# Kernel tuning notes

Hardware: AMD Instinct MI355X
Metric: run time of the kernel (lower is better)

The kernel has to match this reference:

```python
import jax, jax.numpy as jnp
import numpy as np

N_NODES = 50000


def _sage_conv(x, src, dst, W_l, W_r, b, num_nodes):
    # message = x[src]; scatter-mean onto dst (PyG SAGEConv aggr='mean')
    msg = x[src]                                                # [E, C_in]
    agg_sum = jax.ops.segment_sum(msg, dst, num_segments=num_nodes)
    deg = jax.ops.segment_sum(jnp.ones((src.shape[0],), x.dtype), dst,
                              num_segments=num_nodes)
    agg = agg_sum / jnp.maximum(deg, 1.0)[:, None]              # mean, deg clamped to 1
    # lin_l(agg) + lin_r(x); bias lives in lin_l (PyG default)
    return agg @ W_l.T + x @ W_r.T + b


def setup_inputs() -> dict:
    key = jax.random.key(0)
    ks = jax.random.split(key, 8)
    C = 128
    s = 1.0 / np.sqrt(C)
    x = jax.random.normal(ks[0], (N_NODES, C), dtype=jnp.float32)
    edge_index = jax.random.randint(ks[1], (2, 800000), 0, N_NODES, dtype=jnp.int64)
    W1_l = jax.random.uniform(ks[2], (C, C), jnp.float32, -s, s)
    W1_r = jax.random.uniform(ks[3], (C, C), jnp.float32, -s, s)
    b1 = jax.random.uniform(ks[4], (C,), jnp.float32, -s, s)
    W2_l = jax.random.uniform(ks[5], (C, C), jnp.float32, -s, s)
    W2_r = jax.random.uniform(ks[6], (C, C), jnp.float32, -s, s)
    b2 = jax.random.uniform(ks[7], (C,), jnp.float32, -s, s)
    return {"x": x, "edge_index": edge_index,
            "W1_l": W1_l, "W1_r": W1_r, "b1": b1,
            "W2_l": W2_l, "W2_r": W2_r, "b2": b2}


def reference(x, edge_index, W1_l, W1_r, b1, W2_l, W2_r, b2):
    src, dst = edge_index[0], edge_index[1]
    h = _sage_conv(x, src, dst, W1_l, W1_r, b1, N_NODES)
    h = jax.nn.relu(h)  # dropout p=0.0 -> no-op
    out = _sage_conv(h, src, dst, W2_l, W2_r, b2, N_NODES)
    return out
```

## Files before the change

kernel.cpp:

```cpp
#include <hip/hip_runtime.h>

#define NCH 128
#define MAXBKT 512
#define BKT_SHIFT 7
#define BKT_NODES 128
#define BIN_BATCH 1024
#define NHIST 64

typedef __attribute__((ext_vector_type(8))) short bf16x8;
typedef __attribute__((ext_vector_type(4))) float f32x4;

__device__ __forceinline__ unsigned short f2bf_rne(float f) {
  unsigned u = __float_as_uint(f);
  unsigned r = u + 0x7FFF + ((u >> 16) & 1);
  return (unsigned short)(r >> 16);
}

__device__ __forceinline__ void prepW_elem(const float* __restrict__ Wl,
                                           const float* __restrict__ Wr,
                                           unsigned short* __restrict__ WhiF,
                                           unsigned short* __restrict__ WloF, int i) {
  int kc   = i >> 12;
  int r    = i & 4095;
  int nt   = r >> 9;
  int r2   = r & 511;
  int lane = r2 >> 3;
  int e    = r2 & 7;
  int j = nt * 16 + (lane & 15);
  int k = kc * 32 + (lane >> 4) * 8 + e;
  float w = (k < 128) ? Wl[j * 128 + k] : Wr[j * 128 + (k - 128)];
  unsigned u = __float_as_uint(w);
  float fhi = __uint_as_float(u & 0xFFFF0000u);
  float flo = w - fhi;
  WhiF[i] = (unsigned short)(u >> 16);
  WloF[i] = (unsigned short)(__float_as_uint(flo) >> 16);
}

__global__ __launch_bounds__(256) void k_hist_prep(
    const int* __restrict__ dst, int* __restrict__ partial,
    const float* __restrict__ x, unsigned short* __restrict__ xbf,
    const float* __restrict__ W1l, const float* __restrict__ W1r,
    const float* __restrict__ W2l, const float* __restrict__ W2r,
    unsigned short* __restrict__ W1hi, unsigned short* __restrict__ W1lo,
    unsigned short* __restrict__ W2hi, unsigned short* __restrict__ W2lo,
    int nE, int n8) {
  int t = threadIdx.x;
  if (blockIdx.x < NHIST) {
    __shared__ int h[MAXBKT];
    h[t] = 0; h[t + 256] = 0;
    __syncthreads();
    for (int e = blockIdx.x * 256 + t; e < nE; e += NHIST * 256)
      atomicAdd(&h[dst[e] >> BKT_SHIFT], 1);
    __syncthreads();
    partial[t * NHIST + blockIdx.x] = h[t];
    partial[(t + 256) * NHIST + blockIdx.x] = h[t + 256];
  } else {
    int i = (blockIdx.x - NHIST) * 256 + t;
    if (i < n8) {
      const float4* p = reinterpret_cast<const float4*>(x + (size_t)i * 8);
      float4 v0 = p[0], v1 = p[1];
      uint4 o;
      o.x = (unsigned)f2bf_rne(v0.x) | ((unsigned)f2bf_rne(v0.y) << 16);
      o.y = (unsigned)f2bf_rne(v0.z) | ((unsigned)f2bf_rne(v0.w) << 16);
      o.z = (unsigned)f2bf_rne(v1.x) | ((unsigned)f2bf_rne(v1.y) << 16);
      o.w = (unsigned)f2bf_rne(v1.z) | ((unsigned)f2bf_rne(v1.w) << 16);
      *reinterpret_cast<uint4*>(xbf + (size_t)i * 8) = o;
    } else {
      int j = i - n8;
      if (j < 32768)       prepW_elem(W1l, W1r, W1hi, W1lo, j);
      else if (j < 65536)  prepW_elem(W2l, W2r, W2hi, W2lo, j - 32768);
    }
  }
}

__global__ __launch_bounds__(512) void k_bktscan(const int* __restrict__ partial,
                                                 int* __restrict__ bktBase,
                                                 int* __restrict__ bktCursor, int nBkt) {
  __shared__ int sc[512];
  int t = threadIdx.x;
  int v = 0;
  const int4* p4 = reinterpret_cast<const int4*>(partial + t * NHIST);
#pragma unroll
  for (int b = 0; b < NHIST / 4; b++) {
    int4 d = p4[b];
    v += d.x + d.y + d.z + d.w;
  }
  sc[t] = v;
  __syncthreads();
  for (int off = 1; off < 512; off <<= 1) {
    int u = (t >= off) ? sc[t - off] : 0;
    __syncthreads();
    sc[t] += u;
    __syncthreads();
  }
  bktBase[t] = sc[t] - v;
  if (t == 511) bktBase[512] = sc[511];
  bktCursor[t] = 0;
}

__global__ __launch_bounds__(256) void k_bin(const int* __restrict__ src,
                                             const int* __restrict__ dst,
                                             const int* __restrict__ bktBase,
                                             int* __restrict__ bktCursor,
                                             unsigned* __restrict__ binned,
                                             int nE, int nBkt) {
  __shared__ int hist[MAXBKT];
  __shared__ int boff[MAXBKT];
  int t = threadIdx.x;
  hist[t] = 0; hist[t + 256] = 0;
  __syncthreads();

  int eb = blockIdx.x * BIN_BATCH;
  unsigned pk[4];
  short bkt[4];
  int rk[4];
#pragma unroll
  for (int i = 0; i < 4; i++) {
    int e = eb + t + i * 256;
    if (e < nE) {
      int s = src[e], d = dst[e];
      bkt[i] = (short)(d >> BKT_SHIFT);
      pk[i] = (unsigned)s | ((unsigned)(d & (BKT_NODES - 1)) << 16);
      rk[i] = atomicAdd(&hist[d >> BKT_SHIFT], 1);
    } else rk[i] = -1;
  }
  __syncthreads();
  for (int i = t; i < nBkt; i += 256)
    boff[i] = hist[i] ? atomicAdd(&bktCursor[i], hist[i]) : 0;
  __syncthreads();
#pragma unroll
  for (int i = 0; i < 4; i++) {
    if (rk[i] >= 0) {
      int b = bkt[i];
      binned[bktBase[b] + boff[b] + rk[i]] = pk[i];
    }
  }
}

__global__ __launch_bounds__(256) void k_build(const unsigned* __restrict__ binned,
                                               const int* __restrict__ bktBase,
                                               int* __restrict__ start,
                                               float* __restrict__ invdeg,
                                               int* __restrict__ srcSorted,
                                               int nN, int nE) {
  __shared__ int cnt[BKT_NODES];
  __shared__ int sc[BKT_NODES];
  __shared__ int cur[BKT_NODES];
  int b = blockIdx.x, t = threadIdx.x;
  int base = b << BKT_SHIFT;
  int e0 = bktBase[b], e1 = bktBase[b + 1];

  if (t < BKT_NODES) { cnt[t] = 0; cur[t] = 0; }
  __syncthreads();
  for (int i = e0 + t; i < e1; i += 256)
    atomicAdd(&cnt[binned[i] >> 16], 1);
  __syncthreads();
  if (t < BKT_NODES) sc[t] = cnt[t];
  __syncthreads();
  for (int off = 1; off < BKT_NODES; off <<= 1) {
    int u = (t < BKT_NODES && t >= off) ? sc[t - off] : 0;
    __syncthreads();
    if (t < BKT_NODES && t >= off) sc[t] += u;
    __syncthreads();
  }
  if (t < BKT_NODES) {
    int n = base + t;
    if (n < nN) {
      start[n] = e0 + sc[t] - cnt[t];
      invdeg[n] = 1.0f / fmaxf((float)cnt[t], 1.0f);
    }
  }
  if (b == 0 && t == 0) start[nN] = nE;
  __syncthreads();
  for (int i = e0 + t; i < e1; i += 256) {
    unsigned p = binned[i];
    int ld = p >> 16;
    int pos = e0 + sc[ld] - cnt[ld] + atomicAdd(&cur[ld], 1);
    srcSorted[pos] = (int)(p & 0xFFFFu);
  }
}

#define ACC8(v)                                          \
  a0 += __uint_as_float((v).x << 16);                    \
  a1 += __uint_as_float((v).x & 0xFFFF0000u);            \
  a2 += __uint_as_float((v).y << 16);                    \
  a3 += __uint_as_float((v).y & 0xFFFF0000u);            \
  a4 += __uint_as_float((v).z << 16);                    \
  a5 += __uint_as_float((v).z & 0xFFFF0000u);            \
  a6 += __uint_as_float((v).w << 16);                    \
  a7 += __uint_as_float((v).w & 0xFFFF0000u);

__global__ __launch_bounds__(256) void k_gather(const unsigned short* __restrict__ xbf,
                                                const int* __restrict__ srcSorted,
                                                const int* __restrict__ start,
                                                const float* __restrict__ invdeg,
                                                unsigned short* __restrict__ aggbf,
                                                int nN) {
  int node = (blockIdx.x * 256 + threadIdx.x) >> 6;
  if (node >= nN) return;
  int lane = threadIdx.x & 63;
  int unit = lane >> 4;
  int ul   = lane & 15;
  const unsigned short* xb = xbf + ul * 8;

  int s0 = start[node], s1 = start[node + 1];
  float a0 = 0.f, a1 = 0.f, a2 = 0.f, a3 = 0.f,
        a4 = 0.f, a5 = 0.f, a6 = 0.f, a7 = 0.f;
  int i = s0 + unit;
  for (; i + 12 < s1; i += 16) {
    int sa = srcSorted[i],     sb = srcSorted[i + 4];
    int sc = srcSorted[i + 8], sd = srcSorted[i + 12];
    uint4 va = *reinterpret_cast<const uint4*>(xb + (size_t)sa * NCH);
    uint4 vb = *reinterpret_cast<const uint4*>(xb + (size_t)sb * NCH);
    uint4 vc = *reinterpret_cast<const uint4*>(xb + (size_t)sc * NCH);
    uint4 vd = *reinterpret_cast<const uint4*>(xb + (size_t)sd * NCH);
    ACC8(va) ACC8(vb) ACC8(vc) ACC8(vd)
  }
  for (; i < s1; i += 4) {
    int s = srcSorted[i];
    uint4 v = *reinterpret_cast<const uint4*>(xb + (size_t)s * NCH);
    ACC8(v)
  }
  a0 += __shfl_xor(a0, 16); a0 += __shfl_xor(a0, 32);
  a1 += __shfl_xor(a1, 16); a1 += __shfl_xor(a1, 32);
  a2 += __shfl_xor(a2, 16); a2 += __shfl_xor(a2, 32);
  a3 += __shfl_xor(a3, 16); a3 += __shfl_xor(a3, 32);
  a4 += __shfl_xor(a4, 16); a4 += __shfl_xor(a4, 32);
  a5 += __shfl_xor(a5, 16); a5 += __shfl_xor(a5, 32);
  a6 += __shfl_xor(a6, 16); a6 += __shfl_xor(a6, 32);
  a7 += __shfl_xor(a7, 16); a7 += __shfl_xor(a7, 32);

  if (lane < 16) {
    float idg = invdeg[node];
    uint4 o;
    o.x = (unsigned)f2bf_rne(a0 * idg) | ((unsigned)f2bf_rne(a1 * idg) << 16);
    o.y = (unsigned)f2bf_rne(a2 * idg) | ((unsigned)f2bf_rne(a3 * idg) << 16);
    o.z = (unsigned)f2bf_rne(a4 * idg) | ((unsigned)f2bf_rne(a5 * idg) << 16);
    o.w = (unsigned)f2bf_rne(a6 * idg) | ((unsigned)f2bf_rne(a7 * idg) << 16);
    *reinterpret_cast<uint4*>(aggbf + (size_t)node * NCH + ul * 8) = o;
  }
}

__global__ __launch_bounds__(256, 3) void k_linear_mfma(
    const unsigned short* __restrict__ aggbf, const unsigned short* __restrict__ xinbf,
    const unsigned short* __restrict__ Whi, const unsigned short* __restrict__ Wlo,
    const float* __restrict__ bias, float* __restrict__ outF,
    unsigned short* __restrict__ outBf, int relu, int nNodes) {
  int t = threadIdx.x;
  int wave = t >> 6;
  int lane = t & 63;
  int l15 = lane & 15;
  int lq  = lane >> 4;
  int r0 = (blockIdx.x * 4 + wave) * 32;

  const bf16x8* WhiV = reinterpret_cast<const bf16x8*>(Whi) + lane;
  const bf16x8* WloV = reinterpret_cast<const bf16x8*>(Wlo) + lane;

  f32x4 accA[8], accB[8];
#pragma unroll
  for (int i = 0; i < 8; i++) {
    accA[i] = (f32x4){0.f, 0.f, 0.f, 0.f};
    accB[i] = (f32x4){0.f, 0.f, 0.f, 0.f};
  }

  int rA = r0 + l15;        if (rA >= nNodes) rA = nNodes - 1;
  int rB = r0 + 16 + l15;   if (rB >= nNodes) rB = nNodes - 1;

#pragma unroll
  for (int kc = 0; kc < 8; kc++) {
    const unsigned short* ab = (kc < 4) ? aggbf : xinbf;
    int k128 = (kc & 3) * 32 + lq * 8;
    bf16x8 aA = *reinterpret_cast<const bf16x8*>(ab + (size_t)rA * NCH + k128);
    bf16x8 aB = *reinterpret_cast<const bf16x8*>(ab + (size_t)rB * NCH + k128);
#pragma unroll
    for (int nt = 0; nt < 8; nt++) {
      int fidx = (kc * 8 + nt) * 64;
      bf16x8 bhi = WhiV[fidx];
      bf16x8 blo = WloV[fidx];
      accA[nt] = __builtin_amdgcn_mfma_f32_16x16x32_bf16(aA, bhi, accA[nt], 0, 0, 0);
      accA[nt] = __builtin_amdgcn_mfma_f32_16x16x32_bf16(aA, blo, accA[nt], 0, 0, 0);
      accB[nt] = __builtin_amdgcn_mfma_f32_16x16x32_bf16(aB, bhi, accB[nt], 0, 0, 0);
      accB[nt] = __builtin_amdgcn_mfma_f32_16x16x32_bf16(aB, blo, accB[nt], 0, 0, 0);
    }
  }

#pragma unroll
  for (int nt = 0; nt < 8; nt++) {
    int col = nt * 16 + l15;
    float bv = bias[col];
#pragma unroll
    for (int i = 0; i < 4; i++) {
      int rowA = r0 + lq * 4 + i;
      if (rowA < nNodes) {
        float v = accA[nt][i] + bv;
        if (relu) v = fmaxf(v, 0.f);
        if (outBf) outBf[(size_t)rowA * NCH + col] = f2bf_rne(v);
        else       outF[(size_t)rowA * NCH + col] = v;
      }
      int rowB = r0 + 16 + lq * 4 + i;
      if (rowB < nNodes) {
        float v = accB[nt][i] + bv;
        if (relu) v = fmaxf(v, 0.f);
        if (outBf) outBf[(size_t)rowB * NCH + col] = f2bf_rne(v);
        else       outF[(size_t)rowB * NCH + col] = v;
      }
    }
  }
}

extern "C" void kernel_launch(void* const* d_in, const int* in_sizes, int n_in,
                              void* d_out, int out_size, void* d_ws, size_t ws_size,
                              hipStream_t stream) {
  const float* x   = (const float*)d_in[0];
  const int*   ei  = (const int*)d_in[1];
  const float* W1l = (const float*)d_in[2];
  const float* W1r = (const float*)d_in[3];
  const float* b1  = (const float*)d_in[4];
  const float* W2l = (const float*)d_in[5];
  const float* W2r = (const float*)d_in[6];
  const float* b2  = (const float*)d_in[7];
  float* out = (float*)d_out;

  const int nE = in_sizes[1] / 2;
  const int nN = in_sizes[0] / NCH;
  const int* src = ei;
  const int* dst = ei + nE;
  const int nBkt = (nN + BKT_NODES - 1) >> BKT_SHIFT;

  size_t bfBytes = (size_t)nN * NCH * sizeof(unsigned short);
  size_t wBytes  = (size_t)128 * 256 * sizeof(unsigned short);
  auto align256 = [](size_t v) { return (v + 255) & ~(size_t)255; };

  char* ws = (char*)d_ws;
  unsigned short* xbf   = (unsigned short*)ws;  ws += bfBytes;
  unsigned short* aggbf = (unsigned short*)ws;  ws += bfBytes;
  unsigned short* hbf   = (unsigned short*)ws;  ws += bfBytes;
  unsigned* binned = (unsigned*)ws;             ws += align256((size_t)nE * sizeof(unsigned));
  int*   srcSorted = (int*)ws;                  ws += align256((size_t)nE * sizeof(int));
  int*   startRow  = (int*)ws;                  ws += align256((size_t)(nN + 1) * sizeof(int));
  float* invdeg    = (float*)ws;                ws += align256((size_t)nN * sizeof(float));
  int*   partial   = (int*)ws;                  ws += (size_t)NHIST * MAXBKT * sizeof(int);
  int*   bktCursor = (int*)ws;                  ws += MAXBKT * sizeof(int);
  int*   bktBase   = (int*)ws;                  ws += align256((MAXBKT + 1) * sizeof(int));
  unsigned short* W1hi = (unsigned short*)ws;   ws += wBytes;
  unsigned short* W1lo = (unsigned short*)ws;   ws += wBytes;
  unsigned short* W2hi = (unsigned short*)ws;   ws += wBytes;
  unsigned short* W2lo = (unsigned short*)ws;   ws += wBytes;

  int n8 = nN * NCH / 8;
  int prepBlocks = (n8 + 2 * 32768) / 256;

  k_hist_prep<<<NHIST + prepBlocks, 256, 0, stream>>>(dst, partial, x, xbf,
                                                      W1l, W1r, W2l, W2r,
                                                      W1hi, W1lo, W2hi, W2lo, nE, n8);
  k_bktscan<<<1, 512, 0, stream>>>(partial, bktBase, bktCursor, nBkt);
  k_bin<<<(nE + BIN_BATCH - 1) / BIN_BATCH, 256, 0, stream>>>(src, dst, bktBase,
                                                              bktCursor, binned, nE, nBkt);
  k_build<<<nBkt, 256, 0, stream>>>(binned, bktBase, startRow, invdeg, srcSorted, nN, nE);

  int gatherBlocks = (nN * 64 + 255) / 256;
  int linBlocks = (nN + 127) / 128;

  k_gather<<<gatherBlocks, 256, 0, stream>>>(xbf, srcSorted, startRow, invdeg, aggbf, nN);
  k_linear_mfma<<<linBlocks, 256, 0, stream>>>(aggbf, xbf, W1hi, W1lo, b1,
                                               nullptr, hbf, 1, nN);

  k_gather<<<gatherBlocks, 256, 0, stream>>>(hbf, srcSorted, startRow, invdeg, aggbf, nN);
  k_linear_mfma<<<linBlocks, 256, 0, stream>>>(aggbf, hbf, W2hi, W2lo, b2,
                                               out, nullptr, 0, nN);
}
```

Baseline: 184.6 us.

## Gather each node with 16 lanes and bin 4096 edges per block

```diff
diff --git a/kernel.cpp b/kernel.cpp
--- a/kernel.cpp
+++ b/kernel.cpp
@@ -4,7 +4,7 @@
 #define MAXBKT 512
 #define BKT_SHIFT 7
 #define BKT_NODES 128
-#define BIN_BATCH 1024
+#define BIN_BATCH 4096
 #define NHIST 64
 
 typedef __attribute__((ext_vector_type(8))) short bf16x8;
@@ -111,11 +111,11 @@
   __syncthreads();
 
   int eb = blockIdx.x * BIN_BATCH;
-  unsigned pk[4];
-  short bkt[4];
-  int rk[4];
-#pragma unroll
-  for (int i = 0; i < 4; i++) {
+  unsigned pk[16];
+  short bkt[16];
+  int rk[16];
+#pragma unroll
+  for (int i = 0; i < 16; i++) {
     int e = eb + t + i * 256;
     if (e < nE) {
       int s = src[e], d = dst[e];
@@ -129,7 +129,7 @@
     boff[i] = hist[i] ? atomicAdd(&bktCursor[i], hist[i]) : 0;
   __syncthreads();
 #pragma unroll
-  for (int i = 0; i < 4; i++) {
+  for (int i = 0; i < 16; i++) {
     if (rk[i] >= 0) {
       int b = bkt[i];
       binned[bktBase[b] + boff[b] + rk[i]] = pk[i];
@@ -196,49 +196,36 @@
                                                 const float* __restrict__ invdeg,
                                                 unsigned short* __restrict__ aggbf,
                                                 int nN) {
-  int node = (blockIdx.x * 256 + threadIdx.x) >> 6;
+  int gid = blockIdx.x * 256 + threadIdx.x;
+  int node = gid >> 4;
   if (node >= nN) return;
-  int lane = threadIdx.x & 63;
-  int unit = lane >> 4;
-  int ul   = lane & 15;
-  const unsigned short* xb = xbf + ul * 8;
-
+  int c = (gid & 15) << 3;
+  const unsigned short* xb = xbf + c;
   int s0 = start[node], s1 = start[node + 1];
   float a0 = 0.f, a1 = 0.f, a2 = 0.f, a3 = 0.f,
         a4 = 0.f, a5 = 0.f, a6 = 0.f, a7 = 0.f;
-  int i = s0 + unit;
-  for (; i + 12 < s1; i += 16) {
-    int sa = srcSorted[i],     sb = srcSorted[i + 4];
-    int sc = srcSorted[i + 8], sd = srcSorted[i + 12];
+  int i = s0;
+  for (; i + 4 <= s1; i += 4) {
+    int sa = srcSorted[i],      sb = srcSorted[i + 1];
+    int sc_ = srcSorted[i + 2], sd = srcSorted[i + 3];
     uint4 va = *reinterpret_cast<const uint4*>(xb + (size_t)sa * NCH);
     uint4 vb = *reinterpret_cast<const uint4*>(xb + (size_t)sb * NCH);
-    uint4 vc = *reinterpret_cast<const uint4*>(xb + (size_t)sc * NCH);
+    uint4 vc = *reinterpret_cast<const uint4*>(xb + (size_t)sc_ * NCH);
     uint4 vd = *reinterpret_cast<const uint4*>(xb + (size_t)sd * NCH);
     ACC8(va) ACC8(vb) ACC8(vc) ACC8(vd)
   }
-  for (; i < s1; i += 4) {
+  for (; i < s1; i++) {
     int s = srcSorted[i];
     uint4 v = *reinterpret_cast<const uint4*>(xb + (size_t)s * NCH);
     ACC8(v)
   }
-  a0 += __shfl_xor(a0, 16); a0 += __shfl_xor(a0, 32);
-  a1 += __shfl_xor(a1, 16); a1 += __shfl_xor(a1, 32);
-  a2 += __shfl_xor(a2, 16); a2 += __shfl_xor(a2, 32);
-  a3 += __shfl_xor(a3, 16); a3 += __shfl_xor(a3, 32);
-  a4 += __shfl_xor(a4, 16); a4 += __shfl_xor(a4, 32);
-  a5 += __shfl_xor(a5, 16); a5 += __shfl_xor(a5, 32);
-  a6 += __shfl_xor(a6, 16); a6 += __shfl_xor(a6, 32);
-  a7 += __shfl_xor(a7, 16); a7 += __shfl_xor(a7, 32);
-
-  if (lane < 16) {
-    float idg = invdeg[node];
-    uint4 o;
-    o.x = (unsigned)f2bf_rne(a0 * idg) | ((unsigned)f2bf_rne(a1 * idg) << 16);
-    o.y = (unsigned)f2bf_rne(a2 * idg) | ((unsigned)f2bf_rne(a3 * idg) << 16);
-    o.z = (unsigned)f2bf_rne(a4 * idg) | ((unsigned)f2bf_rne(a5 * idg) << 16);
-    o.w = (unsigned)f2bf_rne(a6 * idg) | ((unsigned)f2bf_rne(a7 * idg) << 16);
-    *reinterpret_cast<uint4*>(aggbf + (size_t)node * NCH + ul * 8) = o;
-  }
+  float idg = invdeg[node];
+  uint4 o;
+  o.x = (unsigned)f2bf_rne(a0 * idg) | ((unsigned)f2bf_rne(a1 * idg) << 16);
+  o.y = (unsigned)f2bf_rne(a2 * idg) | ((unsigned)f2bf_rne(a3 * idg) << 16);
+  o.z = (unsigned)f2bf_rne(a4 * idg) | ((unsigned)f2bf_rne(a5 * idg) << 16);
+  o.w = (unsigned)f2bf_rne(a6 * idg) | ((unsigned)f2bf_rne(a7 * idg) << 16);
+  *reinterpret_cast<uint4*>(aggbf + (size_t)node * NCH + c) = o;
 }
 
 __global__ __launch_bounds__(256, 3) void k_linear_mfma(
@@ -358,7 +345,7 @@
                                                               bktCursor, binned, nE, nBkt);
   k_build<<<nBkt, 256, 0, stream>>>(binned, bktBase, startRow, invdeg, srcSorted, nN, nE);
 
-  int gatherBlocks = (nN * 64 + 255) / 256;
+  int gatherBlocks = (nN * 16 + 255) / 256;
   int linBlocks = (nN + 127) / 128;
 
   k_gather<<<gatherBlocks, 256, 0, stream>>>(xbf, srcSorted, startRow, invdeg, aggbf, nN);
```

Result: faster. 169.6 us (-8.1%).
